# Kernel tuning notes

Measured on AMD Instinct MI355X. Metric: run time of the kernel, lower is better.

## Reference

```python
import jax, jax.numpy as jnp
import numpy as np

N_NODES = 100000
N_EDGES = 1600000
D_IN = 128
D_HID = 128
LATENT = 64
N_GRAPHS = 512


def setup_inputs() -> dict:
    key = jax.random.key(0)
    ks = jax.random.split(key, 10)
    x = jax.random.normal(ks[0], (N_NODES, D_IN), dtype=jnp.float32)
    edge_index = jax.random.randint(ks[1], (2, N_EDGES), 0, N_NODES, dtype=jnp.int64)
    batch = jnp.sort(jax.random.randint(ks[2], (N_NODES,), 0, N_GRAPHS, dtype=jnp.int64))
    def lin(k, fan_in, fan_out):
        return jax.random.normal(k, (fan_in, fan_out), dtype=jnp.float32) / np.sqrt(fan_in)
    W1 = lin(ks[3], D_IN, D_HID); b1 = jnp.zeros((D_HID,), jnp.float32)
    W2 = lin(ks[4], D_HID, D_HID); b2 = jnp.zeros((D_HID,), jnp.float32)
    W3 = lin(ks[5], D_HID, 2 * LATENT); b3 = jnp.zeros((2 * LATENT,), jnp.float32)
    return {"x": x, "edge_index": edge_index, "batch": batch,
            "W1": W1, "b1": b1, "W2": W2, "b2": b2, "W3": W3, "b3": b3}


def _gcn_norm(edge_index, n_nodes):
    # PyG GCNConv default: add self-loops, symmetric normalization
    loop = jnp.arange(n_nodes, dtype=edge_index.dtype)
    src = jnp.concatenate([edge_index[0], loop])
    dst = jnp.concatenate([edge_index[1], loop])
    deg = jax.ops.segment_sum(jnp.ones_like(dst, dtype=jnp.float32), dst,
                              num_segments=n_nodes)
    dinv = jnp.where(deg > 0, jax.lax.rsqrt(deg), 0.0)
    norm = dinv[src] * dinv[dst]  # [E + N]
    return src, dst, norm


def _gcn_conv(x, W, b, src, dst, norm, n_nodes):
    h = x @ W                               # [N, d_out]
    msg = h[src] * norm[:, None]            # gather + scale, [E+N, d_out]
    agg = jax.ops.segment_sum(msg, dst, num_segments=n_nodes)
    return agg + b


def reference(x, edge_index, batch, W1, b1, W2, b2, W3, b3):
    n = x.shape[0]
    src, dst, norm = _gcn_norm(edge_index, n)
    h = jax.nn.relu(_gcn_conv(x, W1, b1, src, dst, norm, n))
    h = jax.nn.relu(_gcn_conv(h, W2, b2, src, dst, norm, n))
    h = _gcn_conv(h, W3, b3, src, dst, norm, n)
    # scatter_mean over batch ids -> [num_graphs, 2*latent]
    cnt = jax.ops.segment_sum(jnp.ones((n,), jnp.float32), batch,
                              num_segments=N_GRAPHS)
    summed = jax.ops.segment_sum(h, batch, num_segments=N_GRAPHS)
    return summed / jnp.maximum(cnt, 1.0)[:, None]
```

## Files before the change

### kernel.cpp

```cpp
#include <hip/hip_runtime.h>
#include <stdint.h>

typedef unsigned short u16;
typedef unsigned int   u32;

#define N_NODES  100000
#define N_EDGES  1600000
#define DFEAT    128
#define N_GRAPHS 512

#define NBKT   391
#define EPB    8192
#define NBLK_E 196
#define LBUF   8192

typedef float f32x4 __attribute__((ext_vector_type(4)));
typedef short s16x8 __attribute__((ext_vector_type(8)));

__device__ __forceinline__ float bflo(u32 u) { return __uint_as_float(u << 16); }
__device__ __forceinline__ float bfhi(u32 u) { return __uint_as_float(u & 0xffff0000u); }
__device__ __forceinline__ u16 f2bf(float f) {
  u32 u = __float_as_uint(f);
  return (u16)((u + 0x7fffu + ((u >> 16) & 1u)) >> 16);
}
__device__ __forceinline__ u32 pack2(float f0, float f1) {
  return (u32)f2bf(f0) | ((u32)f2bf(f1) << 16);
}

__device__ __forceinline__ int ld_src(const int* ei, int m, int e) {
  return m ? ei[2 * e] : ei[e];
}
__device__ __forceinline__ int ld_dst(const int* ei, int m, int e) {
  return m ? ei[2 * (N_EDGES + e)] : ei[N_EDGES + e];
}

__device__ __forceinline__ int detect_m_block(const int* __restrict__ ei, int* sm) {
  int t = threadIdx.x;
  if (t < 64) {
    int v = ei[2 * t + 1];
    unsigned long long b = __ballot(v != 0);
    if (t == 0) *sm = (b == 0ull) ? 1 : 0;
  }
  __syncthreads();
  return *sm;
}

__global__ __launch_bounds__(256) void histA_k(const int* __restrict__ ei,
                                               int* __restrict__ ghist,
                                               const float* __restrict__ W1,
                                               const float* __restrict__ W2,
                                               const float* __restrict__ W3,
                                               u16* __restrict__ T1, u16* __restrict__ T2,
                                               u16* __restrict__ T3, int* __restrict__ flag) {
  int t = threadIdx.x, b = blockIdx.x;
  if (b >= NBLK_E) {
    int r = b - NBLK_E;
    if (r < 3) {
      const float* W = (r == 0) ? W1 : (r == 1) ? W2 : W3;
      u16* T         = (r == 0) ? T1 : (r == 1) ? T2 : T3;
      for (int i = t; i < DFEAT * DFEAT; i += 256) {
        int n = i >> 7, k = i & 127;
        T[i] = f2bf(W[k * DFEAT + n]);
      }
    } else {
      if (t < 64) {
        int v = ei[2 * t + 1];
        unsigned long long mm = __ballot(v != 0);
        if (t == 0) *flag = (mm == 0ull) ? 1 : 0;
      }
    }
    return;
  }
  __shared__ int sm;
  __shared__ int hist[NBKT];
  int m = detect_m_block(ei, &sm);
  for (int i = t; i < NBKT; i += 256) hist[i] = 0;
  __syncthreads();
  int e0 = b * EPB;
#pragma unroll
  for (int p = 0; p < EPB / 256; p++) {
    int e = e0 + p * 256 + t;
    if (e < N_EDGES) atomicAdd(&hist[ld_dst(ei, m, e) >> 8], 1);
  }
  __syncthreads();
  for (int i = t; i < NBKT; i += 256) ghist[b * NBKT + i] = hist[i];
}

__global__ __launch_bounds__(256) void scanB1_k(int* __restrict__ ghist,
                                                int* __restrict__ gtot) {
  __shared__ int ts[256];
  int t = threadIdx.x, k = blockIdx.x;
  int v = (t < NBLK_E) ? ghist[t * NBKT + k] : 0;
  ts[t] = v;
  for (int off = 1; off < 256; off <<= 1) {
    __syncthreads(); int add = (t >= off) ? ts[t - off] : 0;
    __syncthreads(); ts[t] += add;
  }
  __syncthreads();
  if (t < NBLK_E) ghist[t * NBKT + k] = ts[t] - v;
  if (t == 255) gtot[k] = ts[255];
}

__device__ __forceinline__ void scan_gtot_block(const int* __restrict__ gtot,
                                                int* bb, int* sc) {
  int t = threadIdx.x;
  int v0 = gtot[t];
  sc[t] = v0;
  for (int off = 1; off < 256; off <<= 1) {
    __syncthreads(); int add = (t >= off) ? sc[t - off] : 0;
    __syncthreads(); sc[t] += add;
  }
  __syncthreads();
  bb[t] = sc[t] - v0;
  int base256 = sc[255];
  __syncthreads();
  int v1 = (t < NBKT - 256) ? gtot[256 + t] : 0;
  sc[t] = v1;
  for (int off = 1; off < 256; off <<= 1) {
    __syncthreads(); int add = (t >= off) ? sc[t - off] : 0;
    __syncthreads(); sc[t] += add;
  }
  __syncthreads();
  if (t < NBKT - 256) bb[256 + t] = base256 + sc[t] - v1;
  if (t == 0) bb[NBKT] = N_EDGES;
  __syncthreads();
}

__global__ __launch_bounds__(256) void scatterC_k(const int* __restrict__ ei,
                                                  const int* __restrict__ obase,
                                                  const int* __restrict__ gtot,
                                                  u32* __restrict__ colpk) {
  __shared__ int sm;
  __shared__ int cur[NBKT];
  __shared__ int bb[NBKT + 1];
  __shared__ int sc[256];
  int t = threadIdx.x, b = blockIdx.x;
  int m = detect_m_block(ei, &sm);
  scan_gtot_block(gtot, bb, sc);
  for (int i = t; i < NBKT; i += 256) cur[i] = bb[i] + obase[b * NBKT + i];
  __syncthreads();
  int e0 = b * EPB;
#pragma unroll
  for (int p = 0; p < EPB / 256; p++) {
    int e = e0 + p * 256 + t;
    if (e < N_EDGES) {
      int d = ld_dst(ei, m, e);
      int s = ld_src(ei, m, e);
      int pos = atomicAdd(&cur[d >> 8], 1);
      colpk[pos] = (u32)s | ((u32)(d & 255) << 24);
    }
  }
}

__global__ __launch_bounds__(256) void fillD_k(const int* __restrict__ gtot,
                                               const u32* __restrict__ colpk,
                                               int* __restrict__ colarr,
                                               int* __restrict__ rowptr,
                                               float* __restrict__ dinv) {
  __shared__ int hist[256];
  __shared__ int cur[256];
  __shared__ int lbuf[LBUF];
  __shared__ int bb[NBKT + 1];
  __shared__ int sc[256];
  int t = threadIdx.x, b = blockIdx.x;
  scan_gtot_block(gtot, bb, sc);
  int base = bb[b], end = bb[b + 1], cnt = end - base;
  hist[t] = 0;
  __syncthreads();
  for (int i = t; i < cnt; i += 256) atomicAdd(&hist[colpk[base + i] >> 24], 1);
  __syncthreads();
  int c = hist[t];
  cur[t] = c;
  for (int off = 1; off < 256; off <<= 1) {
    __syncthreads(); int add = (t >= off) ? cur[t - off] : 0;
    __syncthreads(); cur[t] += add;
  }
  __syncthreads();
  int excl = cur[t] - c;
  int node = b * 256 + t;
  if (node < N_NODES) {
    rowptr[node] = base + excl;
    dinv[node] = rsqrtf((float)(c + 1));
  }
  if (b == NBKT - 1 && t == 0) rowptr[N_NODES] = N_EDGES;
  __syncthreads();
  cur[t] = excl;
  __syncthreads();
  for (int i = t; i < cnt; i += 256) {
    u32 v = colpk[base + i];
    int slot = atomicAdd(&cur[v >> 24], 1);
    if (slot < LBUF) lbuf[slot] = (int)(v & 0x00FFFFFFu);
  }
  __syncthreads();
  for (int i = t; i < cnt; i += 256) colarr[base + i] = lbuf[i];
}

#define LP 136
#define GROWS 128

__global__ __launch_bounds__(512, 4) void gemm_scale_k(const void* __restrict__ Xv,
                                                       int x_is_f32,
                                                       const u16* __restrict__ Wt,
                                                       const float* __restrict__ dinv,
                                                       u16* __restrict__ Y, int nrows) {
  __shared__ u16 sW[128 * LP];
  int tid = threadIdx.x;
  int r0 = blockIdx.x * GROWS;

  for (int c = tid; c < 2048; c += 512) {
    int row = c >> 4, off = (c & 15) * 8;
    *(uint4*)(&sW[row * LP + off]) = *(const uint4*)(Wt + row * DFEAT + off);
  }
  __syncthreads();

  int wave = tid >> 6, lane = tid & 63;
  int q = lane >> 4, r = lane & 15;
  int wr0 = wave * 16;
  int arow = r0 + wr0 + r;
  bool rok = (arow < nrows);

  s16x8 a[4];
  if (x_is_f32) {
    const float* Xf = (const float*)Xv + (size_t)arow * DFEAT;
#pragma unroll
    for (int kk = 0; kk < 4; kk++) {
      uint4 u = make_uint4(0, 0, 0, 0);
      if (rok) {
        int k0 = kk * 32 + q * 8;
        float4 v0 = *(const float4*)(Xf + k0);
        float4 v1 = *(const float4*)(Xf + k0 + 4);
        u.x = pack2(v0.x, v0.y); u.y = pack2(v0.z, v0.w);
        u.z = pack2(v1.x, v1.y); u.w = pack2(v1.z, v1.w);
      }
      a[kk] = *(s16x8*)&u;
    }
  } else {
    const u16* Xb = (const u16*)Xv + (size_t)arow * DFEAT;
#pragma unroll
    for (int kk = 0; kk < 4; kk++) {
      uint4 u = make_uint4(0, 0, 0, 0);
      if (rok) u = *(const uint4*)(Xb + kk * 32 + q * 8);
      a[kk] = *(s16x8*)&u;
    }
  }

  f32x4 acc[8];
#pragma unroll
  for (int i = 0; i < 8; i++) acc[i] = (f32x4){0.f, 0.f, 0.f, 0.f};

#pragma unroll
  for (int kk = 0; kk < 4; kk++) {
    int k0 = kk * 32;
#pragma unroll
    for (int nt = 0; nt < 8; nt++) {
      s16x8 b = *(const s16x8*)(&sW[(nt * 16 + r) * LP + k0 + q * 8]);
      acc[nt] = __builtin_amdgcn_mfma_f32_16x16x32_bf16(a[kk], b, acc[nt], 0, 0, 0);
    }
  }

  __syncthreads();
#pragma unroll
  for (int i = 0; i < 4; i++) {
    int row = wr0 + q * 4 + i;
    int grow = r0 + row;
    float dv = (grow < nrows) ? dinv[grow] : 0.0f;
#pragma unroll
    for (int nt = 0; nt < 8; nt++) {
      sW[row * LP + nt * 16 + r] = f2bf(acc[nt][i] * dv);
    }
  }
  __syncthreads();
  for (int c = tid; c < 128 * 16; c += 512) {
    int row = c >> 4, seg = c & 15;
    int grow = r0 + row;
    if (grow < nrows) {
      *(uint4*)(Y + (size_t)grow * DFEAT + seg * 8) = *(const uint4*)(&sW[row * LP + seg * 8]);
    }
  }
}

struct Acc8 {
  float a0, a1, a2, a3, a4, a5, a6, a7;
  __device__ __forceinline__ void add(uint4 v) {
    a0 += bflo(v.x); a1 += bfhi(v.x); a2 += bflo(v.y); a3 += bfhi(v.y);
    a4 += bflo(v.z); a5 += bfhi(v.z); a6 += bflo(v.w); a7 += bfhi(v.w);
  }
};

#define AGG_NB_HALF 3125
#define AGG_GRID    6256

__global__ __launch_bounds__(256) void agg_k(const u32* __restrict__ HS,
                                             const float* __restrict__ dinv,
                                             const int* __restrict__ rowptr,
                                             const int* __restrict__ colidx,
                                             const float* __restrict__ bias,
                                             u32* __restrict__ OUT, int do_relu) {
  int t = threadIdx.x;
  int bid = blockIdx.x;
  int res = bid & 7;
  int half = res >> 2;
  int nb = (bid >> 3) * 4 + (res & 3);
  if (nb >= AGG_NB_HALF) return;

  int node = nb * 32 + (t >> 3);
  int fp = t & 7;
  int cbase = half * 32 + fp * 4;

  int s = rowptr[node], e = rowptr[node + 1];

  Acc8 A;
  uint4 v = *(const uint4*)(HS + (size_t)node * 64 + cbase);
  A.a0 = bflo(v.x); A.a1 = bfhi(v.x); A.a2 = bflo(v.y); A.a3 = bfhi(v.y);
  A.a4 = bflo(v.z); A.a5 = bfhi(v.z); A.a6 = bflo(v.w); A.a7 = bfhi(v.w);

  int j = s;
  for (; j + 4 <= e; j += 4) {
    int i0 = colidx[j], i1 = colidx[j + 1], i2 = colidx[j + 2], i3 = colidx[j + 3];
    uint4 w0 = *(const uint4*)(HS + (size_t)i0 * 64 + cbase);
    uint4 w1 = *(const uint4*)(HS + (size_t)i1 * 64 + cbase);
    uint4 w2 = *(const uint4*)(HS + (size_t)i2 * 64 + cbase);
    uint4 w3 = *(const uint4*)(HS + (size_t)i3 * 64 + cbase);
    A.add(w0); A.add(w1); A.add(w2); A.add(w3);
  }
  for (; j < e; j++) {
    int i0 = colidx[j];
    uint4 w0 = *(const uint4*)(HS + (size_t)i0 * 64 + cbase);
    A.add(w0);
  }

  float dv = dinv[node];
  float4 b0 = *(const float4*)(bias + cbase * 2);
  float4 b1 = *(const float4*)(bias + cbase * 2 + 4);
  float r0 = A.a0 * dv + b0.x, r1 = A.a1 * dv + b0.y;
  float r2 = A.a2 * dv + b0.z, r3 = A.a3 * dv + b0.w;
  float r4 = A.a4 * dv + b1.x, r5 = A.a5 * dv + b1.y;
  float r6 = A.a6 * dv + b1.z, r7 = A.a7 * dv + b1.w;
  if (do_relu) {
    r0 = fmaxf(r0, 0.f); r1 = fmaxf(r1, 0.f); r2 = fmaxf(r2, 0.f); r3 = fmaxf(r3, 0.f);
    r4 = fmaxf(r4, 0.f); r5 = fmaxf(r5, 0.f); r6 = fmaxf(r6, 0.f); r7 = fmaxf(r7, 0.f);
  }
  uint4 o;
  o.x = pack2(r0, r1); o.y = pack2(r2, r3); o.z = pack2(r4, r5); o.w = pack2(r6, r7);
  *(uint4*)(OUT + (size_t)node * 64 + cbase) = o;
}

__device__ __forceinline__ int lower_bound_i(const int* a, int n, int key, int shift) {
  int lo = 0, hi = n;
  while (lo < hi) {
    int mid = (lo + hi) >> 1;
    if (a[mid << shift] < key) lo = mid + 1; else hi = mid;
  }
  return lo;
}

__global__ __launch_bounds__(256) void pool_k(const u32* __restrict__ H,
                                              const int* __restrict__ batch,
                                              const int* __restrict__ flag,
                                              float* __restrict__ OUT) {
  int g = blockIdx.x;
  int m = *flag;
  int lo = lower_bound_i(batch, N_NODES, g, m);
  int hi = lower_bound_i(batch, N_NODES, g + 1, m);
  int cnt = hi - lo;
  int d2 = threadIdx.x & 63;
  int half = threadIdx.x >> 6;
  float a0 = 0.f, a1 = 0.f;
  for (int row = lo + half; row < hi; row += 4) {
    u32 v = H[(size_t)row * 64 + d2];
    a0 += bflo(v); a1 += bfhi(v);
  }
  __shared__ float red0[256], red1[256];
  red0[threadIdx.x] = a0; red1[threadIdx.x] = a1;
  __syncthreads();
  if (threadIdx.x < 64) {
    float s0 = red0[d2] + red0[d2 + 64] + red0[d2 + 128] + red0[d2 + 192];
    float s1 = red1[d2] + red1[d2 + 64] + red1[d2 + 128] + red1[d2 + 192];
    float inv = 1.0f / fmaxf((float)cnt, 1.0f);
    OUT[g * DFEAT + 2 * d2]     = s0 * inv;
    OUT[g * DFEAT + 2 * d2 + 1] = s1 * inv;
  }
}


extern "C" void kernel_launch(void* const* d_in, const int* in_sizes, int n_in,
                              void* d_out, int out_size, void* d_ws, size_t ws_size,
                              hipStream_t stream) {
  const float* x   = (const float*)d_in[0];
  const int* ei    = (const int*)d_in[1];
  const int* batch = (const int*)d_in[2];
  const float* W1  = (const float*)d_in[3];
  const float* b1  = (const float*)d_in[4];
  const float* W2  = (const float*)d_in[5];
  const float* b2  = (const float*)d_in[6];
  const float* W3  = (const float*)d_in[7];
  const float* b3  = (const float*)d_in[8];
  float* out = (float*)d_out;

  char* p = (char*)d_ws;
  size_t off = 0;
  auto carve = [&](size_t bytes) -> void* {
    void* q = p + off;
    off = (off + bytes + 255) & ~(size_t)255;
    return q;
  };
  int*   flag   = (int*)carve(256);
  int*   ghist  = (int*)carve((size_t)NBLK_E * NBKT * 4);
  int*   gtot   = (int*)carve(NBKT * 4);
  int*   rowptr = (int*)carve((N_NODES + 1) * 4);
  float* dinv   = (float*)carve(N_NODES * 4);
  u32*   colpk  = (u32*)carve((size_t)N_EDGES * 4);
  int*   colarr = (int*)carve((size_t)N_EDGES * 4);
  u16*   Wt1    = (u16*)carve(DFEAT * DFEAT * 2);
  u16*   Wt2    = (u16*)carve(DFEAT * DFEAT * 2);
  u16*   Wt3    = (u16*)carve(DFEAT * DFEAT * 2);
  u32*   bufA   = (u32*)carve((size_t)N_NODES * 64 * 4);
  u32*   bufB   = (u32*)carve((size_t)N_NODES * 64 * 4);
  (void)ws_size;

  histA_k<<<NBLK_E + 4, 256, 0, stream>>>(ei, ghist, W1, W2, W3, Wt1, Wt2, Wt3, flag);
  scanB1_k<<<NBKT, 256, 0, stream>>>(ghist, gtot);
  scatterC_k<<<NBLK_E, 256, 0, stream>>>(ei, ghist, gtot, colpk);
  fillD_k<<<NBKT, 256, 0, stream>>>(gtot, colpk, colarr, rowptr, dinv);

  const int GB = (N_NODES + GROWS - 1) / GROWS;

  gemm_scale_k<<<GB, 512, 0, stream>>>((const void*)x, 1, Wt1, dinv, (u16*)bufA, N_NODES);
  agg_k<<<AGG_GRID, 256, 0, stream>>>(bufA, dinv, rowptr, colarr, b1, bufB, 1);
  gemm_scale_k<<<GB, 512, 0, stream>>>((const void*)bufB, 0, Wt2, dinv, (u16*)bufA, N_NODES);
  agg_k<<<AGG_GRID, 256, 0, stream>>>(bufA, dinv, rowptr, colarr, b2, bufB, 1);
  gemm_scale_k<<<GB, 512, 0, stream>>>((const void*)bufB, 0, Wt3, dinv, (u16*)bufA, N_NODES);
  agg_k<<<AGG_GRID, 256, 0, stream>>>(bufA, dinv, rowptr, colarr, b3, bufB, 0);
  pool_k<<<N_GRAPHS, 256, 0, stream>>>(bufB, batch, flag, out);
}
```

Before: 383.4 us.

## Store node features in 16-column slabs so aggregation gathers hit a compact region

Hidden-feature buffers change from row-major [N,128] bf16 to eight column slabs of [N,16]. Each aggregation block now handles one slab for 128 nodes, so its random neighbour gathers touch a 3.2MB region that is more likely to stay in cache. The GEMM, aggregation and pooling kernels are all rewritten to read and write this layout, and nontemporal stores and index loads are added. The cost is that each gather now moves only 32 bytes per edge per slab, so there are more small requests in total and the rowptr and colidx arrays are read eight times.

```diff
diff --git a/kernel.cpp b/kernel.cpp
--- a/kernel.cpp
+++ b/kernel.cpp
@@ -14,8 +14,11 @@
 #define NBLK_E 196
 #define LBUF   8192
 
+#define SL_STRIDE ((size_t)N_NODES * 16)
+
 typedef float f32x4 __attribute__((ext_vector_type(4)));
 typedef short s16x8 __attribute__((ext_vector_type(8)));
+typedef unsigned int u32x4 __attribute__((ext_vector_type(4)));
 
 __device__ __forceinline__ float bflo(u32 u) { return __uint_as_float(u << 16); }
 __device__ __forceinline__ float bfhi(u32 u) { return __uint_as_float(u & 0xffff0000u); }
@@ -25,6 +28,10 @@
 }
 __device__ __forceinline__ u32 pack2(float f0, float f1) {
   return (u32)f2bf(f0) | ((u32)f2bf(f1) << 16);
+}
+__device__ __forceinline__ void nt_store16(void* p, uint4 v) {
+  u32x4 w; w.x = v.x; w.y = v.y; w.z = v.z; w.w = v.w;
+  __builtin_nontemporal_store(w, (u32x4*)p);
 }
 
 __device__ __forceinline__ int ld_src(const int* ei, int m, int e) {
@@ -43,6 +50,15 @@
   }
   __syncthreads();
   return *sm;
+}
+
+__device__ __forceinline__ int lower_bound_i(const int* a, int n, int key, int shift) {
+  int lo = 0, hi = n;
+  while (lo < hi) {
+    int mid = (lo + hi) >> 1;
+    if (a[mid << shift] < key) lo = mid + 1; else hi = mid;
+  }
+  return lo;
 }
 
 __global__ __launch_bounds__(256) void histA_k(const int* __restrict__ ei,
@@ -197,6 +213,7 @@
 
 #define LP 136
 #define GROWS 128
+#define GB1   782
 
 __global__ __launch_bounds__(512, 4) void gemm_scale_k(const void* __restrict__ Xv,
                                                        int x_is_f32,
@@ -235,11 +252,15 @@
       a[kk] = *(s16x8*)&u;
     }
   } else {
-    const u16* Xb = (const u16*)Xv + (size_t)arow * DFEAT;
+    const u16* Xb = (const u16*)Xv;
+    int hh = q & 1;
 #pragma unroll
     for (int kk = 0; kk < 4; kk++) {
       uint4 u = make_uint4(0, 0, 0, 0);
-      if (rok) u = *(const uint4*)(Xb + kk * 32 + q * 8);
+      if (rok) {
+        int sidx = kk * 2 + (q >> 1);
+        u = *(const uint4*)(Xb + (size_t)sidx * SL_STRIDE + (size_t)arow * 16 + hh * 8);
+      }
       a[kk] = *(s16x8*)&u;
     }
   }
@@ -253,8 +274,8 @@
     int k0 = kk * 32;
 #pragma unroll
     for (int nt = 0; nt < 8; nt++) {
-      s16x8 b = *(const s16x8*)(&sW[(nt * 16 + r) * LP + k0 + q * 8]);
-      acc[nt] = __builtin_amdgcn_mfma_f32_16x16x32_bf16(a[kk], b, acc[nt], 0, 0, 0);
+      s16x8 bfrag = *(const s16x8*)(&sW[(nt * 16 + r) * LP + k0 + q * 8]);
+      acc[nt] = __builtin_amdgcn_mfma_f32_16x16x32_bf16(a[kk], bfrag, acc[nt], 0, 0, 0);
     }
   }
 
@@ -270,91 +291,88 @@
     }
   }
   __syncthreads();
-  for (int c = tid; c < 128 * 16; c += 512) {
-    int row = c >> 4, seg = c & 15;
+  for (int c = tid; c < 1024; c += 512) {
+    int sidx = c >> 7, row = c & 127;
     int grow = r0 + row;
     if (grow < nrows) {
-      *(uint4*)(Y + (size_t)grow * DFEAT + seg * 8) = *(const uint4*)(&sW[row * LP + seg * 8]);
-    }
-  }
-}
-
-struct Acc8 {
-  float a0, a1, a2, a3, a4, a5, a6, a7;
-  __device__ __forceinline__ void add(uint4 v) {
-    a0 += bflo(v.x); a1 += bfhi(v.x); a2 += bflo(v.y); a3 += bfhi(v.y);
-    a4 += bflo(v.z); a5 += bfhi(v.z); a6 += bflo(v.w); a7 += bfhi(v.w);
-  }
-};
-
-#define AGG_NB_HALF 3125
-#define AGG_GRID    6256
-
-__global__ __launch_bounds__(256) void agg_k(const u32* __restrict__ HS,
+      const u16* src = &sW[row * LP + sidx * 16];
+      u16* dst = Y + (size_t)sidx * SL_STRIDE + (size_t)grow * 16;
+      nt_store16(dst, *(const uint4*)src);
+      nt_store16(dst + 8, *(const uint4*)(src + 8));
+    }
+  }
+}
+
+#define AGG_CHUNKS 782
+#define AGG_GRID   (AGG_CHUNKS * 8)
+
+__global__ __launch_bounds__(256) void agg_k(const u16* __restrict__ HS,
                                              const float* __restrict__ dinv,
                                              const int* __restrict__ rowptr,
                                              const int* __restrict__ colidx,
                                              const float* __restrict__ bias,
-                                             u32* __restrict__ OUT, int do_relu) {
-  int t = threadIdx.x;
-  int bid = blockIdx.x;
-  int res = bid & 7;
-  int half = res >> 2;
-  int nb = (bid >> 3) * 4 + (res & 3);
-  if (nb >= AGG_NB_HALF) return;
-
-  int node = nb * 32 + (t >> 3);
-  int fp = t & 7;
-  int cbase = half * 32 + fp * 4;
-
-  int s = rowptr[node], e = rowptr[node + 1];
-
-  Acc8 A;
-  uint4 v = *(const uint4*)(HS + (size_t)node * 64 + cbase);
-  A.a0 = bflo(v.x); A.a1 = bfhi(v.x); A.a2 = bflo(v.y); A.a3 = bfhi(v.y);
-  A.a4 = bflo(v.z); A.a5 = bfhi(v.z); A.a6 = bflo(v.w); A.a7 = bfhi(v.w);
-
-  int j = s;
-  for (; j + 4 <= e; j += 4) {
-    int i0 = colidx[j], i1 = colidx[j + 1], i2 = colidx[j + 2], i3 = colidx[j + 3];
-    uint4 w0 = *(const uint4*)(HS + (size_t)i0 * 64 + cbase);
-    uint4 w1 = *(const uint4*)(HS + (size_t)i1 * 64 + cbase);
-    uint4 w2 = *(const uint4*)(HS + (size_t)i2 * 64 + cbase);
-    uint4 w3 = *(const uint4*)(HS + (size_t)i3 * 64 + cbase);
-    A.add(w0); A.add(w1); A.add(w2); A.add(w3);
-  }
-  for (; j < e; j++) {
-    int i0 = colidx[j];
-    uint4 w0 = *(const uint4*)(HS + (size_t)i0 * 64 + cbase);
-    A.add(w0);
+                                             u16* __restrict__ OUT, int do_relu) {
+  int t = threadIdx.x, bid = blockIdx.x;
+  int s = bid & 7;
+  int chunk = bid >> 3;
+  int node = chunk * 128 + (t >> 1);
+  if (node >= N_NODES) return;
+  int h = t & 1;
+  const u16* base = HS + (size_t)s * SL_STRIDE + h * 8;
+
+  int rs = rowptr[node], re = rowptr[node + 1];
+
+  float a0, a1, a2, a3, a4, a5, a6, a7;
+  {
+    uint4 v = *(const uint4*)(base + (size_t)node * 16);
+    a0 = bflo(v.x); a1 = bfhi(v.x); a2 = bflo(v.y); a3 = bfhi(v.y);
+    a4 = bflo(v.z); a5 = bfhi(v.z); a6 = bflo(v.w); a7 = bfhi(v.w);
+  }
+
+  int j = rs;
+  for (; j + 4 <= re; j += 4) {
+    int i0 = __builtin_nontemporal_load(colidx + j);
+    int i1 = __builtin_nontemporal_load(colidx + j + 1);
+    int i2 = __builtin_nontemporal_load(colidx + j + 2);
+    int i3 = __builtin_nontemporal_load(colidx + j + 3);
+    uint4 w0 = *(const uint4*)(base + (size_t)i0 * 16);
+    uint4 w1 = *(const uint4*)(base + (size_t)i1 * 16);
+    uint4 w2 = *(const uint4*)(base + (size_t)i2 * 16);
+    uint4 w3 = *(const uint4*)(base + (size_t)i3 * 16);
+    a0 += bflo(w0.x) + bflo(w1.x) + bflo(w2.x) + bflo(w3.x);
+    a1 += bfhi(w0.x) + bfhi(w1.x) + bfhi(w2.x) + bfhi(w3.x);
+    a2 += bflo(w0.y) + bflo(w1.y) + bflo(w2.y) + bflo(w3.y);
+    a3 += bfhi(w0.y) + bfhi(w1.y) + bfhi(w2.y) + bfhi(w3.y);
+    a4 += bflo(w0.z) + bflo(w1.z) + bflo(w2.z) + bflo(w3.z);
+    a5 += bfhi(w0.z) + bfhi(w1.z) + bfhi(w2.z) + bfhi(w3.z);
+    a6 += bflo(w0.w) + bflo(w1.w) + bflo(w2.w) + bflo(w3.w);
+    a7 += bfhi(w0.w) + bfhi(w1.w) + bfhi(w2.w) + bfhi(w3.w);
+  }
+  for (; j < re; j++) {
+    int i0 = __builtin_nontemporal_load(colidx + j);
+    uint4 w0 = *(const uint4*)(base + (size_t)i0 * 16);
+    a0 += bflo(w0.x); a1 += bfhi(w0.x); a2 += bflo(w0.y); a3 += bfhi(w0.y);
+    a4 += bflo(w0.z); a5 += bfhi(w0.z); a6 += bflo(w0.w); a7 += bfhi(w0.w);
   }
 
   float dv = dinv[node];
-  float4 b0 = *(const float4*)(bias + cbase * 2);
-  float4 b1 = *(const float4*)(bias + cbase * 2 + 4);
-  float r0 = A.a0 * dv + b0.x, r1 = A.a1 * dv + b0.y;
-  float r2 = A.a2 * dv + b0.z, r3 = A.a3 * dv + b0.w;
-  float r4 = A.a4 * dv + b1.x, r5 = A.a5 * dv + b1.y;
-  float r6 = A.a6 * dv + b1.z, r7 = A.a7 * dv + b1.w;
+  const float* bp = bias + s * 16 + h * 8;
+  float4 b0 = *(const float4*)bp;
+  float4 b1 = *(const float4*)(bp + 4);
+  float r0 = a0 * dv + b0.x, r1 = a1 * dv + b0.y;
+  float r2 = a2 * dv + b0.z, r3 = a3 * dv + b0.w;
+  float r4 = a4 * dv + b1.x, r5 = a5 * dv + b1.y;
+  float r6 = a6 * dv + b1.z, r7 = a7 * dv + b1.w;
   if (do_relu) {
     r0 = fmaxf(r0, 0.f); r1 = fmaxf(r1, 0.f); r2 = fmaxf(r2, 0.f); r3 = fmaxf(r3, 0.f);
     r4 = fmaxf(r4, 0.f); r5 = fmaxf(r5, 0.f); r6 = fmaxf(r6, 0.f); r7 = fmaxf(r7, 0.f);
   }
   uint4 o;
   o.x = pack2(r0, r1); o.y = pack2(r2, r3); o.z = pack2(r4, r5); o.w = pack2(r6, r7);
-  *(uint4*)(OUT + (size_t)node * 64 + cbase) = o;
-}
-
-__device__ __forceinline__ int lower_bound_i(const int* a, int n, int key, int shift) {
-  int lo = 0, hi = n;
-  while (lo < hi) {
-    int mid = (lo + hi) >> 1;
-    if (a[mid << shift] < key) lo = mid + 1; else hi = mid;
-  }
-  return lo;
-}
-
-__global__ __launch_bounds__(256) void pool_k(const u32* __restrict__ H,
+  nt_store16(OUT + (size_t)s * SL_STRIDE + (size_t)node * 16 + h * 8, o);
+}
+
+__global__ __launch_bounds__(256) void pool_k(const u16* __restrict__ H,
                                               const int* __restrict__ batch,
                                               const int* __restrict__ flag,
                                               float* __restrict__ OUT) {
@@ -365,9 +383,10 @@
   int cnt = hi - lo;
   int d2 = threadIdx.x & 63;
   int half = threadIdx.x >> 6;
+  const u16* base = H + (size_t)(d2 >> 3) * SL_STRIDE + (d2 & 7) * 2;
   float a0 = 0.f, a1 = 0.f;
   for (int row = lo + half; row < hi; row += 4) {
-    u32 v = H[(size_t)row * 64 + d2];
+    u32 v = *(const u32*)(base + (size_t)row * 16);
     a0 += bflo(v); a1 += bfhi(v);
   }
   __shared__ float red0[256], red1[256];
@@ -414,8 +433,8 @@
   u16*   Wt1    = (u16*)carve(DFEAT * DFEAT * 2);
   u16*   Wt2    = (u16*)carve(DFEAT * DFEAT * 2);
   u16*   Wt3    = (u16*)carve(DFEAT * DFEAT * 2);
-  u32*   bufA   = (u32*)carve((size_t)N_NODES * 64 * 4);
-  u32*   bufB   = (u32*)carve((size_t)N_NODES * 64 * 4);
+  u16*   bufA   = (u16*)carve(8 * SL_STRIDE * 2);
+  u16*   bufB   = (u16*)carve(8 * SL_STRIDE * 2);
   (void)ws_size;
 
   histA_k<<<NBLK_E + 4, 256, 0, stream>>>(ei, ghist, W1, W2, W3, Wt1, Wt2, Wt3, flag);
@@ -423,13 +442,11 @@
   scatterC_k<<<NBLK_E, 256, 0, stream>>>(ei, ghist, gtot, colpk);
   fillD_k<<<NBKT, 256, 0, stream>>>(gtot, colpk, colarr, rowptr, dinv);
 
-  const int GB = (N_NODES + GROWS - 1) / GROWS;
-
-  gemm_scale_k<<<GB, 512, 0, stream>>>((const void*)x, 1, Wt1, dinv, (u16*)bufA, N_NODES);
+  gemm_scale_k<<<GB1, 512, 0, stream>>>((const void*)x, 1, Wt1, dinv, bufA, N_NODES);
   agg_k<<<AGG_GRID, 256, 0, stream>>>(bufA, dinv, rowptr, colarr, b1, bufB, 1);
-  gemm_scale_k<<<GB, 512, 0, stream>>>((const void*)bufB, 0, Wt2, dinv, (u16*)bufA, N_NODES);
+  gemm_scale_k<<<GB1, 512, 0, stream>>>((const void*)bufB, 0, Wt2, dinv, bufA, N_NODES);
   agg_k<<<AGG_GRID, 256, 0, stream>>>(bufA, dinv, rowptr, colarr, b2, bufB, 1);
-  gemm_scale_k<<<GB, 512, 0, stream>>>((const void*)bufB, 0, Wt3, dinv, (u16*)bufA, N_NODES);
+  gemm_scale_k<<<GB1, 512, 0, stream>>>((const void*)bufB, 0, Wt3, dinv, bufA, N_NODES);
   agg_k<<<AGG_GRID, 256, 0, stream>>>(bufA, dinv, rowptr, colarr, b3, bufB, 0);
   pool_k<<<N_GRAPHS, 256, 0, stream>>>(bufB, batch, flag, out);
 }
```

Result: slower. 610.2 us (+59.2%).
